# Kernel tuning notes

Measured on AMD Instinct MI355X. Metric: run time of the kernel, lower is better.

Reference implementation:

```python
import jax, jax.numpy as jnp
import numpy as np

BETA = 0.99
TOL = 1e-4
MAX_ITER = 1000
EPS = 1e-3
B, N, HF, HV, KV = 65536, 32, 25, 128, 8


def fhat(x, fp):
    W1, b1, W2, b2, W3, b3 = fp
    h = jax.nn.softplus(x @ W1 + b1)
    h = jax.nn.softplus(h @ W2 + b2)
    return h @ W3 + b3  # (B,1,N)


def V(z, vp):
    # Lyapunov function: V(z) = ||g(z)-g(0)||^2 + eps*||z||^2 ; V(0)=0, V>0 elsewhere.
    W1, b1, W2, b2, W3, b3 = vp
    def mlp(u):
        h = jax.nn.softplus(u @ W1 + b1)
        h = jax.nn.softplus(h @ W2 + b2)
        return h @ W3 + b3
    h = mlp(z)
    h0 = mlp(jnp.zeros((1, 1, z.shape[-1]), z.dtype))
    return (jnp.sum((h - h0) ** 2, axis=-1, keepdims=True)
            + EPS * jnp.sum(z * z, axis=-1, keepdims=True))  # (B,1,1)


def newton_F(fhatx, target, gamma, vp):
    # F = gamma - (V(fhatx*gamma)-target)/dV_dgamma  (newton_iter.forward)
    Vg, dV = jax.jvp(lambda g: V(fhatx * g, vp), (gamma,), (jnp.ones_like(gamma),))
    return gamma - (Vg - target) / dV


def solve_gamma(fhatx, target, vp):
    # Vectorized masked Newton + bisection (rootfind_train.forward).
    gamma = jnp.ones((fhatx.shape[0], 1, 1), fhatx.dtype)
    e1 = jnp.zeros_like(gamma)
    e2 = jnp.ones_like(gamma)
    active = (V(fhatx, vp) - target) > 0.0  # samples needing rootfind

    def cond(s):
        return jnp.logical_and(jnp.any(s[3]), s[4] < MAX_ITER)

    def body(s):
        gamma, e1, e2, m, it = s
        # Newton step on active, unconverged samples
        newt = newton_F(fhatx, target, gamma, vp)
        gamma = jnp.where(m, newt, gamma)
        # bisection backup where Newton left [e1,e2] (or produced non-finite)
        m_bisec = m & ((gamma < e1) | (gamma > e2) | ~jnp.isfinite(gamma))
        a = 0.5 * (e1 + e2)
        s_a = jnp.sign(V(fhatx * a, vp) - target)
        s_1 = jnp.sign(V(fhatx * e1, vp) - target)
        s_2 = jnp.sign(V(fhatx * e2, vp) - target)
        e2 = jnp.where(m_bisec & (s_a * s_1 < 0), a, e2)
        e1 = jnp.where(m_bisec & (s_a * s_2 < 0), a, e1)
        gamma = jnp.where(m_bisec, a, gamma)
        m = active & (jnp.abs(V(fhatx * gamma, vp) - target) > TOL)
        return (gamma, e1, e2, m, it + 1)

    gamma = jax.lax.while_loop(cond, body, (gamma, e1, e2, active, jnp.int32(0)))[0]
    return gamma


@jax.jit
def _forward(x, fp, vp):
    fhatx = fhat(x, fp)
    target = BETA * V(x, vp)
    viol = V(fhatx, vp) > target  # these go through rootfind; rest pass through fhat
    gamma = solve_gamma(fhatx, target, vp)
    return jnp.where(viol, fhatx * gamma, fhatx)


def setup_inputs() -> dict:
    key = jax.random.key(0)
    ks = jax.random.split(key, 13)
    def w(k, shape, fan):
        return jax.random.normal(k, shape, jnp.float32) / np.float32(np.sqrt(fan))
    return {
        'x': jax.random.normal(ks[0], (B, 1, N), jnp.float32),
        'f_W1': w(ks[1], (N, HF), N), 'f_b1': jnp.zeros((HF,), jnp.float32),
        'f_W2': w(ks[2], (HF, HF), HF), 'f_b2': jnp.zeros((HF,), jnp.float32),
        'f_W3': w(ks[3], (HF, N), HF), 'f_b3': jnp.zeros((N,), jnp.float32),
        'v_W1': w(ks[4], (N, HV), N), 'v_b1': jnp.zeros((HV,), jnp.float32),
        'v_W2': w(ks[5], (HV, HV), HV), 'v_b2': jnp.zeros((HV,), jnp.float32),
        'v_W3': w(ks[6], (HV, KV), HV), 'v_b3': jnp.zeros((KV,), jnp.float32),
    }


def reference(x, f_W1, f_b1, f_W2, f_b2, f_W3, f_b3,
              v_W1, v_b1, v_W2, v_b2, v_W3, v_b3):
    fp = (f_W1, f_b1, f_W2, f_b2, f_W3, f_b3)
    vp = (v_W1, v_b1, v_W2, v_b2, v_W3, v_b3)
    return _forward(x, fp, vp)
```

## Files before the change

kernel.cpp:

```cpp
#include <hip/hip_runtime.h>
#include <math.h>

#define BETA_C   0.99f
#define TOL_C    1e-4f
#define ACC_C    2e-3f
#define BRK_C    2e-3f
#define FORCE_C  6
#define MAXIT_C  1000
#define EPS_C    1e-3f
#define BN       65536
#define NN       32
#define HFD      25
#define HVD      128
#define KVD      8
#define G        16
#define GPB      16
#define SGPB     16
#define SBLK     256
#define NQBLK    768


typedef __attribute__((ext_vector_type(8))) short bf16x8;
typedef __attribute__((ext_vector_type(8))) unsigned short u16x8;
typedef __attribute__((ext_vector_type(4))) float f32x4;

__device__ __forceinline__ void wsync() {
    __builtin_amdgcn_wave_barrier();
    __threadfence_block();
    __builtin_amdgcn_wave_barrier();
}

__device__ __forceinline__ float sp_(float x) {
    return fmaxf(x, 0.f) + log1pf(expf(-fabsf(x)));
}
__device__ __forceinline__ float spf_(float x) {
    return fmaxf(x, 0.f) + __logf(1.f + __expf(-fabsf(x)));
}
__device__ __forceinline__ float sgn_(float d) {
    return (d > 0.f) ? 1.f : ((d < 0.f) ? -1.f : 0.f);
}
__device__ __forceinline__ unsigned short f2bf(float f) {
    unsigned int u = __float_as_uint(f);
    u += 0x7FFFu + ((u >> 16) & 1u);
    return (unsigned short)(u >> 16);
}
__device__ __forceinline__ float bf2f(unsigned short u) {
    return __uint_as_float(((unsigned int)u) << 16);
}

__device__ __forceinline__ void aw_st(unsigned short* aw, int row, int col, float v) {
    const int b = (row * 64 + col * 2) ^ ((row & 3) << 4);
    *(unsigned short*)((char*)aw + b) = f2bf(v);
}
__device__ __forceinline__ bf16x8 aw_ld(const unsigned short* aw, int row, int k) {
    const int b = (row * 64 + k * 2) ^ ((row & 3) << 4);
    return *(const bf16x8*)((const char*)aw + b);
}
__device__ __forceinline__ void hw_st(unsigned short* hw, int row, int col, float v) {
    const int b = (row * 256 + col * 2) ^ ((row & 7) << 4);
    *(unsigned short*)((char*)hw + b) = f2bf(v);
}
__device__ __forceinline__ bf16x8 hw_ld(const unsigned short* hw, int row, int k) {
    const int b = (row * 256 + k * 2) ^ ((row & 7) << 4);
    return *(const bf16x8*)((const char*)hw + b);
}

__device__ __forceinline__ void veval2_sec(
    const int gl, const float (&uA)[8], const float (&uB)[8],
    const float gA, const float gB,
    float2* h1q, const float n2A, const float n2B,
    const float (&b1v)[8], const float (&b2v)[8], const float (&d0c)[8],
    const unsigned short* w2L, const unsigned short* __restrict__ w3s,
    float& VA, float& VB)
{
    const int k0 = gl * 8;
#pragma unroll
    for (int j = 0; j < 8; ++j) {
        const float preA = fmaf(gA, uA[j], b1v[j]);
        const float preB = fmaf(gB, uB[j], b1v[j]);
        h1q[(j << 4) | gl] = make_float2(spf_(preA), spf_(preB));
    }
    wsync();
    float aA[8], aB[8];
#pragma unroll
    for (int j = 0; j < 8; ++j) { aA[j] = 0.f; aB[j] = 0.f; }
#pragma unroll 4
    for (int k = 0; k < HVD; ++k) {
        const float2 q = h1q[((k & 7) << 4) | (k >> 3)];
        const u16x8 wv = *(const u16x8*)(w2L + k * HVD + k0);
#pragma unroll
        for (int j = 0; j < 8; ++j) {
            const float w = bf2f(wv[j]);
            aA[j] = fmaf(q.x, w, aA[j]);
            aB[j] = fmaf(q.y, w, aB[j]);
        }
    }
    wsync();
    float oA[KVD], oB[KVD];
#pragma unroll
    for (int c = 0; c < KVD; ++c) { oA[c] = 0.f; oB[c] = 0.f; }
#pragma unroll
    for (int j = 0; j < 8; ++j) {
        const float h2A = spf_(aA[j] + b2v[j]);
        const float h2B = spf_(aB[j] + b2v[j]);
        const u16x8 w3v = *(const u16x8*)(w3s + (k0 + j) * KVD);
#pragma unroll
        for (int c = 0; c < 8; ++c) {
            const float w3 = bf2f(w3v[c]);
            oA[c] = fmaf(h2A, w3, oA[c]);
            oB[c] = fmaf(h2B, w3, oB[c]);
        }
    }
#pragma unroll
    for (int m = 1; m < G; m <<= 1) {
#pragma unroll
        for (int c = 0; c < KVD; ++c) {
            oA[c] += __shfl_xor(oA[c], m);
            oB[c] += __shfl_xor(oB[c], m);
        }
    }
    float vvA = 0.f, vvB = 0.f;
#pragma unroll
    for (int c = 0; c < KVD; ++c) {
        const float eA = oA[c] + d0c[c];
        const float eB = oB[c] + d0c[c];
        vvA = fmaf(eA, eA, vvA);
        vvB = fmaf(eB, eB, vvB);
    }
    VA = vvA + EPS_C * gA * gA * n2A;
    VB = vvB + EPS_C * gB * gB * n2B;
}

__global__ __launch_bounds__(256, 2) void k_wprep(
    const float* __restrict__ vW1, const float* __restrict__ vW2,
    const float* __restrict__ vW3,
    const float* __restrict__ vb1, const float* __restrict__ vb2,
    const float* __restrict__ vb3,
    unsigned short* __restrict__ w1b, unsigned short* __restrict__ w2b,
    unsigned short* __restrict__ w3b,
    unsigned short* __restrict__ w2s, unsigned short* __restrict__ w3s,
    float* __restrict__ h0g)
{
    if (blockIdx.x == 32) {
        __shared__ float h1s[HVD];
        __shared__ float h2p[2][HVD];
        __shared__ float h2s[HVD];
        __shared__ float o3p[16][KVD + 1];
        const int t = threadIdx.x;
        if (t < HVD) h1s[t] = sp_(vb1[t]);
        __syncthreads();
        {
            const int j = t & 127, half = t >> 7;
            float a = half ? 0.f : vb2[j];
            const int kb = half * 64;
            for (int k = 0; k < 64; ++k)
                a = fmaf(h1s[kb + k], vW2[(kb + k) * HVD + j], a);
            h2p[half][j] = a;
        }
        __syncthreads();
        if (t < HVD) h2s[t] = sp_(h2p[0][t] + h2p[1][t]);
        __syncthreads();
        if (t < 128) {
            const int c = t & 7, ch = t >> 3;
            float a = 0.f;
            for (int k = ch * 8; k < ch * 8 + 8; ++k)
                a = fmaf(h2s[k], vW3[k * KVD + c], a);
            o3p[ch][c] = a;
        }
        __syncthreads();
        if (t < KVD) {
            float acc = vb3[t];
            for (int ch = 0; ch < 16; ++ch) acc += o3p[ch][t];
            h0g[t] = acc;
        }
        return;
    }
    const int t = blockIdx.x * 256 + threadIdx.x;
    const int nth = 32 * 256;
    for (int i = t; i < HVD * NN; i += nth) {
        const int col = i >> 5, k = i & 31;
        w1b[i] = f2bf(vW1[k * HVD + col]);
    }
    for (int i = t; i < HVD * HVD; i += nth) {
        const int col = i >> 7, k = i & 127;
        w2b[i] = f2bf(vW2[k * HVD + col]);
    }
    for (int i = t; i < 16 * HVD; i += nth) {
        const int c = i >> 7, k = i & 127;
        w3b[i] = (c < KVD) ? f2bf(vW3[k * KVD + c]) : (unsigned short)0;
    }
    for (int i = t; i < HVD * HVD; i += nth)
        w2s[i] = f2bf(vW2[i]);
    for (int i = t; i < HVD * KVD; i += nth)
        w3s[i] = f2bf(vW3[i]);
}

__global__ __launch_bounds__(256, 2) void k_setup(
    const float* __restrict__ x_g,
    const float* __restrict__ fW1, const float* __restrict__ fb1,
    const float* __restrict__ fW2, const float* __restrict__ fb2,
    const float* __restrict__ fW3, const float* __restrict__ fb3,
    const float* __restrict__ vb1, const float* __restrict__ vb2,
    const float* __restrict__ vb3,
    const unsigned short* __restrict__ w1b,
    const unsigned short* __restrict__ w2b,
    const unsigned short* __restrict__ w3b,
    const float* __restrict__ h0g,
    float* __restrict__ out,
    int* __restrict__ cnt, int* __restrict__ list, float* __restrict__ tgt,
    float* __restrict__ vfb)
{
    __shared__ float2 xs[GPB][NN + 1];
    __shared__ float2 fh1[GPB][HFD + 1];
    __shared__ float2 fh2[GPB][HFD + 1];
    __shared__ __align__(16) unsigned short abf[4][16 * 32];
    __shared__ __align__(16) unsigned short hbf[4][16 * HVD];
    __shared__ int wcnt[4];
    __shared__ int bbase;

    const int tid = threadIdx.x;
    const int gi = tid >> 4;
    const int gl = tid & (G - 1);
    const int w  = tid >> 6;
    const int l  = tid & 63;
    const int q  = l >> 4;
    const int cc = l & 15;
    const int sb = (blockIdx.x * GPB + gi) * 2;
    const int s0 = sb, s1 = sb + 1;
    unsigned short* aw = abf[w];
    unsigned short* hw = hbf[w];

    const float xa0 = x_g[(size_t)s0 * NN + gl];
    const float xa1 = x_g[(size_t)s0 * NN + gl + 16];
    const float xb0 = x_g[(size_t)s1 * NN + gl];
    const float xb1 = x_g[(size_t)s1 * NN + gl + 16];
    xs[gi][gl]      = make_float2(xa0, xb0);
    xs[gi][gl + 16] = make_float2(xa1, xb1);
    const int r0 = 4 * q;
    aw_st(aw, r0,     gl,      xa0); aw_st(aw, r0,     gl + 16, xa1);
    aw_st(aw, r0 + 2, gl,      xb0); aw_st(aw, r0 + 2, gl + 16, xb1);
    wsync();

    float fA0, fA1, fB0, fB1;
    for (int uu = gl; uu < HFD; uu += G) {
        float a0 = fb1[uu];
        float a1 = a0;
#pragma unroll
        for (int i = 0; i < NN; ++i) {
            const float2 xv2 = xs[gi][i];
            const float wv = fW1[i * HFD + uu];
            a0 = fmaf(xv2.x, wv, a0);
            a1 = fmaf(xv2.y, wv, a1);
        }
        fh1[gi][uu] = make_float2(spf_(a0), spf_(a1));
    }
    wsync();
    for (int uu = gl; uu < HFD; uu += G) {
        float a0 = fb2[uu];
        float a1 = a0;
#pragma unroll
        for (int i = 0; i < HFD; ++i) {
            const float2 h = fh1[gi][i];
            const float wv = fW2[i * HFD + uu];
            a0 = fmaf(h.x, wv, a0);
            a1 = fmaf(h.y, wv, a1);
        }
        fh2[gi][uu] = make_float2(spf_(a0), spf_(a1));
    }
    wsync();
    {
        float A0 = fb3[gl], A1 = fb3[gl + 16];
        float B0 = A0,      B1 = A1;
#pragma unroll
        for (int i = 0; i < HFD; ++i) {
            const float2 h = fh2[gi][i];
            const float wa = fW3[i * NN + gl];
            const float wb = fW3[i * NN + gl + 16];
            A0 = fmaf(h.x, wa, A0); A1 = fmaf(h.x, wb, A1);
            B0 = fmaf(h.y, wa, B0); B1 = fmaf(h.y, wb, B1);
        }
        out[(size_t)s0 * NN + gl]      = A0;
        out[(size_t)s0 * NN + gl + 16] = A1;
        out[(size_t)s1 * NN + gl]      = B0;
        out[(size_t)s1 * NN + gl + 16] = B1;
        aw_st(aw, r0 + 1, gl, A0); aw_st(aw, r0 + 1, gl + 16, A1);
        aw_st(aw, r0 + 3, gl, B0); aw_st(aw, r0 + 3, gl + 16, B1);
        fA0 = A0; fA1 = A1; fB0 = B0; fB1 = B1;
    }
    wsync();

    float p0 = fmaf(xa0, xa0, xa1 * xa1);
    float p1 = fmaf(fA0, fA0, fA1 * fA1);
    float p2 = fmaf(xb0, xb0, xb1 * xb1);
    float p3 = fmaf(fB0, fB0, fB1 * fB1);
#pragma unroll
    for (int m = 1; m < G; m <<= 1) {
        p0 += __shfl_xor(p0, m); p1 += __shfl_xor(p1, m);
        p2 += __shfl_xor(p2, m); p3 += __shfl_xor(p3, m);
    }

    float b1v[8], b2v[8];
#pragma unroll
    for (int n = 0; n < 8; ++n) {
        b1v[n] = vb1[n * 16 + cc];
        b2v[n] = vb2[n * 16 + cc];
    }

    const int kq = (l >> 4) * 8;
    const f32x4 zf = {0.f, 0.f, 0.f, 0.f};

    const bf16x8 afr = aw_ld(aw, cc, kq);
    f32x4 acc1[8];
#pragma unroll
    for (int n = 0; n < 8; ++n) {
        const bf16x8 bfr = *(const bf16x8*)(w1b + (n * 16 + cc) * 32 + kq);
        acc1[n] = __builtin_amdgcn_mfma_f32_16x16x32_bf16(afr, bfr, zf, 0, 0, 0);
    }
#pragma unroll
    for (int n = 0; n < 8; ++n) {
#pragma unroll
        for (int r = 0; r < 4; ++r)
            hw_st(hw, r0 + r, n * 16 + cc, spf_(acc1[n][r] + b1v[n]));
    }
    wsync();

    f32x4 acc2[8];
#pragma unroll
    for (int n = 0; n < 8; ++n) acc2[n] = zf;
#pragma unroll
    for (int c = 0; c < 4; ++c) {
        const bf16x8 a2f = hw_ld(hw, cc, c * 32 + kq);
#pragma unroll
        for (int n = 0; n < 8; ++n) {
            const bf16x8 b2f = *(const bf16x8*)(w2b + (n * 16 + cc) * HVD + c * 32 + kq);
            acc2[n] = __builtin_amdgcn_mfma_f32_16x16x32_bf16(a2f, b2f, acc2[n], 0, 0, 0);
        }
    }
    wsync();
#pragma unroll
    for (int n = 0; n < 8; ++n) {
#pragma unroll
        for (int r = 0; r < 4; ++r)
            hw_st(hw, r0 + r, n * 16 + cc, spf_(acc2[n][r] + b2v[n]));
    }
    wsync();

    f32x4 acc3 = zf;
#pragma unroll
    for (int c = 0; c < 4; ++c) {
        const bf16x8 a3f = hw_ld(hw, cc, c * 32 + kq);
        const bf16x8 b3f = *(const bf16x8*)(w3b + cc * HVD + c * 32 + kq);
        acc3 = __builtin_amdgcn_mfma_f32_16x16x32_bf16(a3f, b3f, acc3, 0, 0, 0);
    }

    const float d0 = (cc < KVD) ? (vb3[cc] - h0g[cc]) : 0.f;
    float s_[4];
#pragma unroll
    for (int r = 0; r < 4; ++r) {
        const float e = (cc < KVD) ? (acc3[r] + d0) : 0.f;
        s_[r] = e * e;
    }
#pragma unroll
    for (int m = 1; m < G; m <<= 1) {
#pragma unroll
        for (int r = 0; r < 4; ++r) s_[r] += __shfl_xor(s_[r], m);
    }
    const float Vx0 = s_[0] + EPS_C * p0;
    const float Vf0 = s_[1] + EPS_C * p1;
    const float Vx1 = s_[2] + EPS_C * p2;
    const float Vf1 = s_[3] + EPS_C * p3;

    const float t0 = BETA_C * Vx0;
    const float t1 = BETA_C * Vx1;
    const bool act0 = (Vf0 - t0) > 0.f;
    const bool act1 = (Vf1 - t1) > 0.f;

    const bool lead = (gl == 0 && act0) || (gl == 1 && act1);
    unsigned long long bal = __ballot(lead);
    const int lane = threadIdx.x & 63, wv = threadIdx.x >> 6;
    const int rank = __popcll(bal & ((1ull << lane) - 1ull));
    if (lane == 0) wcnt[wv] = __popcll(bal);
    __syncthreads();
    if (threadIdx.x == 0) {
        int tot = 0;
        for (int i = 0; i < 4; ++i) { int c = wcnt[i]; wcnt[i] = tot; tot += c; }
        bbase = atomicAdd(cnt, tot);
    }
    __syncthreads();
    if (lead) {
        const int p = bbase + wcnt[wv] + rank;
        list[p] = (gl == 0) ? s0 : s1;
        tgt[p]  = (gl == 0) ? t0 : t1;
        vfb[p]  = (gl == 0) ? Vf0 : Vf1;
    }
}

__global__ __launch_bounds__(SBLK, 2) void k_solve(
    const float* __restrict__ vW1, const float* __restrict__ vb1,
    const unsigned short* __restrict__ w2s, const float* __restrict__ vb2,
    const unsigned short* __restrict__ w3s, const float* __restrict__ vb3,
    const float* __restrict__ h0g,
    float* __restrict__ out,
    const int* __restrict__ cnt, const int* __restrict__ list,
    const float* __restrict__ tgt, const float* __restrict__ vfb,
    int* __restrict__ qhead)
{
    __shared__ __align__(16) unsigned short w2L[HVD * HVD];
    __shared__ __align__(8) float2 h1s[SGPB][HVD];

    {
        const uint4* s2 = (const uint4*)w2s;
        uint4* d2 = (uint4*)w2L;
        for (int i = threadIdx.x; i < (HVD * HVD) / 8; i += SBLK) d2[i] = s2[i];
    }
    __syncthreads();

    const int gi = threadIdx.x >> 4;
    const int gl = threadIdx.x & (G - 1);
    const int n  = *cnt;
    float2* h1q = h1s[gi];
    const int lead = threadIdx.x & 48;

    const int k0 = gl * 8;
    float b1v[8], b2v[8], d0c[8];
    {
        const float4 a = *(const float4*)(vb1 + k0);
        const float4 b = *(const float4*)(vb1 + k0 + 4);
        b1v[0]=a.x; b1v[1]=a.y; b1v[2]=a.z; b1v[3]=a.w;
        b1v[4]=b.x; b1v[5]=b.y; b1v[6]=b.z; b1v[7]=b.w;
        const float4 c = *(const float4*)(vb2 + k0);
        const float4 d = *(const float4*)(vb2 + k0 + 4);
        b2v[0]=c.x; b2v[1]=c.y; b2v[2]=c.z; b2v[3]=c.w;
        b2v[4]=d.x; b2v[5]=d.y; b2v[6]=d.z; b2v[7]=d.w;
#pragma unroll
        for (int cix = 0; cix < KVD; ++cix) d0c[cix] = vb3[cix] - h0g[cix];
    }

    int sA, sB; float tgA, tgB, fA0, fA1, fB0, fB1, n2A, n2B;
    float uA[8], uB[8];
    float gA, e1A, e2A, vA1, vA2, pgA, pvA;
    float gB, e1B, e2B, vB1, vB2, pgB, pvB;
    bool doneA, doneB;
    int itA, itB, obhA, obhB;

    auto grab = [&]() -> bool {
        int v = 0;
        if (gl == 0) v = atomicAdd(qhead, 2);
        v = __shfl(v, lead);
        if (v >= n) return false;
        const bool hasB = (v + 1) < n;
        sA = list[v]; tgA = tgt[v];
        const float vfA = vfb[v];
        float vfB;
        if (hasB) { sB = list[v + 1]; tgB = tgt[v + 1]; vfB = vfb[v + 1]; }
        else      { sB = sA;          tgB = tgA;        vfB = vfA; }
        fA0 = out[(size_t)sA * NN + gl];
        fA1 = out[(size_t)sA * NN + gl + 16];
        fB0 = out[(size_t)sB * NN + gl];
        fB1 = out[(size_t)sB * NN + gl + 16];
        float pa = fmaf(fA0, fA0, fA1 * fA1);
        float pb = fmaf(fB0, fB0, fB1 * fB1);
#pragma unroll
        for (int m = 1; m < G; m <<= 1) {
            pa += __shfl_xor(pa, m);
            pb += __shfl_xor(pb, m);
        }
        n2A = pa; n2B = pb;
#pragma unroll
        for (int j = 0; j < 8; ++j) { uA[j] = 0.f; uB[j] = 0.f; }
#pragma unroll
        for (int i = 0; i < NN; ++i) {
            const int src = lead + (i & 15);
            const float qx = __shfl((i < 16) ? fA0 : fA1, src);
            const float qy = __shfl((i < 16) ? fB0 : fB1, src);
            const float4 wa = *(const float4*)(vW1 + i * HVD + k0);
            const float4 wb = *(const float4*)(vW1 + i * HVD + k0 + 4);
            uA[0] = fmaf(qx, wa.x, uA[0]); uA[1] = fmaf(qx, wa.y, uA[1]);
            uA[2] = fmaf(qx, wa.z, uA[2]); uA[3] = fmaf(qx, wa.w, uA[3]);
            uA[4] = fmaf(qx, wb.x, uA[4]); uA[5] = fmaf(qx, wb.y, uA[5]);
            uA[6] = fmaf(qx, wb.z, uA[6]); uA[7] = fmaf(qx, wb.w, uA[7]);
            uB[0] = fmaf(qy, wa.x, uB[0]); uB[1] = fmaf(qy, wa.y, uB[1]);
            uB[2] = fmaf(qy, wa.z, uB[2]); uB[3] = fmaf(qy, wa.w, uB[3]);
            uB[4] = fmaf(qy, wb.x, uB[4]); uB[5] = fmaf(qy, wb.y, uB[5]);
            uB[6] = fmaf(qy, wb.z, uB[6]); uB[7] = fmaf(qy, wb.w, uB[7]);
        }
        gA = sqrtf(tgA / vfA); e1A = 0.f; e2A = 1.f; vA1 = 0.f; vA2 = vfA;
        pgA = 1.f; pvA = vfA;
        gB = sqrtf(tgB / vfB); e1B = 0.f; e2B = 1.f; vB1 = 0.f; vB2 = vfB;
        pgB = 1.f; pvB = vfB;
        doneA = false; itA = 0; obhA = 0;
        doneB = !hasB; itB = 0; obhB = 0;
        return true;
    };
    if (!grab()) return;

    auto step = [&](bool& done, float& gamma, float& pg, float& pv,
                    float& e1, float& e2, float& v_e1, float& v_e2,
                    int& it, int& obh,
                    const float vp, const float target,
                    const int s, const float f0, const float f1) {
        if (done) return;
        if (fabsf(vp - target) <= TOL_C || (e2 - e1) <= BRK_C) {
            out[(size_t)s * NN + gl]      = f0 * gamma;
            out[(size_t)s * NN + gl + 16] = f1 * gamma;
            done = true;
            return;
        }
        const float sa = sgn_(vp - target);
        const float s1 = sgn_(v_e1 - target);
        if (sa * s1 < 0.f) { e2 = gamma; v_e2 = vp; }
        else               { e1 = gamma; v_e1 = vp; }
        ++it;
        const float newt = gamma - (vp - target) * (gamma - pg) / (vp - pv);
        pg = gamma; pv = vp;
        if (it < FORCE_C && newt >= e1 && newt <= e2) {
            if (fabsf(newt - gamma) <= ACC_C) {
                out[(size_t)s * NN + gl]      = f0 * newt;
                out[(size_t)s * NN + gl + 16] = f1 * newt;
                done = true;
                return;
            }
            gamma = newt;
        } else if (newt > e2 && e2 >= 1.0f) {
            if (++obh >= 2) {
                out[(size_t)s * NN + gl]      = f0;
                out[(size_t)s * NN + gl + 16] = f1;
                done = true;
                return;
            }
            gamma = 0.5f * (e1 + e2);
        } else {
            if (it & 1) {
                gamma = 0.5f * (e1 + e2);
            } else {
                const float fr0 = (target - v_e1) / (v_e2 - v_e1);
                const float fr = fminf(fmaxf(fr0, 0.1f), 0.9f);
                gamma = fmaf(fr, e2 - e1, e1);
            }
        }
        if (it >= MAXIT_C) {
            out[(size_t)s * NN + gl]      = f0 * gamma;
            out[(size_t)s * NN + gl + 16] = f1 * gamma;
            done = true;
        }
    };

    for (;;) {
        float vpA, vpB;
        veval2_sec(gl, uA, uB, gA, gB, h1q, n2A, n2B,
                   b1v, b2v, d0c, w2L, w3s, vpA, vpB);
        step(doneA, gA, pgA, pvA, e1A, e2A, vA1, vA2, itA, obhA, vpA, tgA, sA, fA0, fA1);
        step(doneB, gB, pgB, pvB, e1B, e2B, vB1, vB2, itB, obhB, vpB, tgB, sB, fB0, fB1);
        if (doneA && doneB) {
            if (!grab()) break;
        }
    }
}

extern "C" void kernel_launch(void* const* d_in, const int* in_sizes, int n_in,
                              void* d_out, int out_size, void* d_ws, size_t ws_size,
                              hipStream_t stream)
{
    const float* x   = (const float*)d_in[0];
    const float* fW1 = (const float*)d_in[1];
    const float* fb1 = (const float*)d_in[2];
    const float* fW2 = (const float*)d_in[3];
    const float* fb2 = (const float*)d_in[4];
    const float* fW3 = (const float*)d_in[5];
    const float* fb3 = (const float*)d_in[6];
    const float* vW1 = (const float*)d_in[7];
    const float* vb1 = (const float*)d_in[8];
    const float* vW2 = (const float*)d_in[9];
    const float* vb2 = (const float*)d_in[10];
    const float* vW3 = (const float*)d_in[11];
    const float* vb3 = (const float*)d_in[12];
    float* out = (float*)d_out;

    char* ws = (char*)d_ws;
    int*   cnt   = (int*)ws;
    int*   qhead = (int*)(ws + 4);
    float* h0g   = (float*)(ws + 64);
    int*   list  = (int*)(ws + 128);
    float* tgt   = (float*)(ws + 128 + (size_t)BN * 4);
    float* vfb   = (float*)(ws + 128 + (size_t)BN * 8);
    unsigned short* w1b = (unsigned short*)(ws + 128 + (size_t)BN * 12);
    unsigned short* w2b = w1b + HVD * NN;
    unsigned short* w3b = w2b + HVD * HVD;
    unsigned short* w2s = w3b + 16 * HVD;
    unsigned short* w3s = w2s + HVD * HVD;

    hipMemsetAsync(ws, 0, 8, stream);

    hipLaunchKernelGGL(k_wprep, dim3(33), dim3(256), 0, stream,
                       vW1, vW2, vW3, vb1, vb2, vb3,
                       w1b, w2b, w3b, w2s, w3s, h0g);

    hipLaunchKernelGGL(k_setup, dim3(BN / (GPB * 2)), dim3(256), 0, stream,
                       x, fW1, fb1, fW2, fb2, fW3, fb3,
                       vb1, vb2, vb3, w1b, w2b, w3b,
                       h0g, out, cnt, list, tgt, vfb);

    hipLaunchKernelGGL(k_solve, dim3(NQBLK), dim3(SBLK), 0, stream,
                       vW1, vb1, w2s, vb2, w3s, vb3,
                       h0g, out, cnt, list, tgt, vfb, qhead);
}
```

Measured before the change: 290.0 us.

## Use both probe slots on one sample when its partner finishes

When one of the two per-group sample slots finishes while the other still runs, the remaining sample is copied into both slots. Each iteration then evaluates two points, a clamped false-position point and the midpoint, and shrinks the bracket from both results. This is meant to stop the second evaluation lane idling while waiting for a new sample to be grabbed, so tail samples converge in fewer iterations. It also clamps the work-list count and writes to the buffer size, adding branching and more complex control flow to the solve loop.

New measurement: 374.6 us. 1.29x slower.

```diff
diff --git a/kernel.cpp b/kernel.cpp
--- a/kernel.cpp
+++ b/kernel.cpp
@@ -389,9 +389,11 @@
     __syncthreads();
     if (lead) {
         const int p = bbase + wcnt[wv] + rank;
-        list[p] = (gl == 0) ? s0 : s1;
-        tgt[p]  = (gl == 0) ? t0 : t1;
-        vfb[p]  = (gl == 0) ? Vf0 : Vf1;
+        if (p < BN) {
+            list[p] = (gl == 0) ? s0 : s1;
+            tgt[p]  = (gl == 0) ? t0 : t1;
+            vfb[p]  = (gl == 0) ? Vf0 : Vf1;
+        }
     }
 }
 
@@ -417,7 +419,8 @@
 
     const int gi = threadIdx.x >> 4;
     const int gl = threadIdx.x & (G - 1);
-    const int n  = *cnt;
+    int n = *cnt;
+    if (n > BN) n = BN;
     float2* h1q = h1s[gi];
     const int lead = threadIdx.x & 48;
 
@@ -545,14 +548,71 @@
         }
     };
 
+    auto dual_probes = [&]() {
+        const float w = e2B - e1B;
+        const float fr0 = (tgB - vB1) / (vB2 - vB1);
+        const float fr = fminf(fmaxf(fr0, 0.1f), 0.9f);
+        float gf = fmaf(fr, w, e1B);
+        const float gm = fmaf(0.5f, w, e1B);
+        if (fabsf(gf - gm) < 0.05f * w)
+            gf = fmaf((fr < 0.5f) ? 0.25f : 0.75f, w, e1B);
+        gA = gf; gB = gm;
+    };
+
+    int dual = 0;
     for (;;) {
         float vpA, vpB;
         veval2_sec(gl, uA, uB, gA, gB, h1q, n2A, n2B,
                    b1v, b2v, d0c, w2L, w3s, vpA, vpB);
-        step(doneA, gA, pgA, pvA, e1A, e2A, vA1, vA2, itA, obhA, vpA, tgA, sA, fA0, fA1);
-        step(doneB, gB, pgB, pvB, e1B, e2B, vB1, vB2, itB, obhB, vpB, tgB, sB, fB0, fB1);
-        if (doneA && doneB) {
-            if (!grab()) break;
+        if (!dual) {
+            step(doneA, gA, pgA, pvA, e1A, e2A, vA1, vA2, itA, obhA, vpA, tgA, sA, fA0, fA1);
+            step(doneB, gB, pgB, pvB, e1B, e2B, vB1, vB2, itB, obhB, vpB, tgB, sB, fB0, fB1);
+            if (doneA && doneB) {
+                if (!grab()) break;
+                continue;
+            }
+            if (doneA != doneB) {
+                if (doneB) {
+#pragma unroll
+                    for (int j = 0; j < 8; ++j) uB[j] = uA[j];
+                    n2B = n2A; tgB = tgA; sB = sA; fB0 = fA0; fB1 = fA1;
+                    e1B = e1A; e2B = e2A; vB1 = vA1; vB2 = vA2; itB = itA;
+                } else {
+#pragma unroll
+                    for (int j = 0; j < 8; ++j) uA[j] = uB[j];
+                    n2A = n2B;
+                }
+                dual = 1;
+                dual_probes();
+            }
+        } else {
+            float g1 = gA, v1 = vpA, g2 = gB, v2 = vpB;
+            if (g1 > g2) { float t_; t_ = g1; g1 = g2; g2 = t_;
+                           t_ = v1; v1 = v2; v2 = t_; }
+            bool fin = false; float gout = 0.f;
+            if (fabsf(v1 - tgB) <= TOL_C)      { fin = true; gout = g1; }
+            else if (fabsf(v2 - tgB) <= TOL_C) { fin = true; gout = g2; }
+            else {
+                const float s1 = sgn_(v1 - tgB);
+                const float s2 = sgn_(v2 - tgB);
+                const float sE = sgn_(vB1 - tgB);
+                if (s1 * sE < 0.f)      { e2B = g1; vB2 = v1; }
+                else if (s2 * s1 < 0.f) { e1B = g1; vB1 = v1;
+                                          e2B = g2; vB2 = v2; }
+                else                    { e1B = g2; vB1 = v2; }
+                ++itB;
+                if ((e2B - e1B) <= BRK_C || itB >= MAXIT_C) {
+                    fin = true; gout = 0.5f * (e1B + e2B);
+                }
+            }
+            if (fin) {
+                out[(size_t)sB * NN + gl]      = fB0 * gout;
+                out[(size_t)sB * NN + gl + 16] = fB1 * gout;
+                if (!grab()) break;
+                dual = 0;
+                continue;
+            }
+            dual_probes();
         }
     }
 }
```
